# Optimization experiments

Hardware: AMD Instinct MI355X
Metric: run time of the kernel (lower is better)

The kernel has to match this reference:

```python
import jax, jax.numpy as jnp
import numpy as np

NUM_EXPERTS = 8
TOP_K = 2
HIDDEN = 1024
INTER_TOTAL = 8192  # intermediate_size * experts_per_rank
B, S = 2, 2048


def setup_inputs() -> dict:
    key = jax.random.key(0)
    k1, k2, k3, k4, k5, k6 = jax.random.split(key, 6)
    T = B * S
    x = jax.random.normal(k1, (B, S, HIDDEN), dtype=jnp.float32)
    scores = jax.random.uniform(k2, (T, NUM_EXPERTS), dtype=jnp.float32)
    expert_weights = jax.random.uniform(k3, (T, TOP_K), dtype=jnp.float32)
    top_experts = jax.random.randint(k4, (T, TOP_K), 0, NUM_EXPERTS, dtype=jnp.int32)
    w1 = jax.random.normal(k5, (HIDDEN, INTER_TOTAL), dtype=jnp.float32) * 0.02
    w2 = jax.random.normal(k6, (INTER_TOTAL, HIDDEN), dtype=jnp.float32) * 0.02
    return {"x": x, "scores": scores, "expert_weights": expert_weights,
            "top_experts": top_experts, "w1": w1, "w2": w2}


def reference(x, scores, expert_weights, top_experts, w1, w2):
    # forward_once with expert_parallel_size == 1 (dropless MoE dispatch/combine).
    in_shape = x.shape
    T = in_shape[0] * in_shape[1]
    H = in_shape[-1]
    x_flat = x.reshape(T, H)

    flat_experts = top_experts.reshape(-1)          # [T*top_k]
    flat_weights = expert_weights.reshape(-1)       # [T*top_k]

    # ops.sort: stable radix sort of routed copies by expert id
    order = jnp.argsort(flat_experts, stable=True)  # "indices"
    token_idx = order // TOP_K                      # source token per sorted slot

    # padded_gather: bucket tokens per expert (padding rows are zeros and
    # pass through the bias-free MLP as zeros, so they never affect output)
    xg = x_flat[token_idx]                          # [T*top_k, H]

    # MLP: w1 -> gelu(tanh approx) -> w2
    h = jax.nn.gelu(xg @ w1, approximate=True)      # [T*top_k, inter*E]
    y = h @ w2                                      # [T*top_k, H]

    # padded_scatter: weighted combine back to token order
    w_sorted = flat_weights[order]
    out = jnp.zeros((T, H), dtype=x.dtype).at[token_idx].add(w_sorted[:, None] * y)
    return out.reshape(in_shape)
```

## Files before the change

kernel.cpp:

```cpp
#include <hip/hip_runtime.h>
#include <hip/hip_bf16.h>
#include <math.h>

#define HID 1024
#define INTER 8192
#define TT 4096

typedef __bf16 bf16x8 __attribute__((ext_vector_type(8)));
typedef float f32x4 __attribute__((ext_vector_type(4)));

__device__ __forceinline__ void gll16(const void* g, void* l) {
    __builtin_amdgcn_global_load_lds(
        (const __attribute__((address_space(1))) void*)g,
        (__attribute__((address_space(3))) void*)l, 16, 0, 0);
}

template <int OFF>
__device__ __forceinline__ bf16x8 ds_read128o(unsigned addr) {
    bf16x8 r;
    asm volatile("ds_read_b128 %0, %1 offset:%c2" : "=v"(r) : "v"(addr), "i"(OFF));
    return r;
}

__global__ void k_prep(const float* __restrict__ x, const float* __restrict__ ew,
                       __hip_bfloat16* __restrict__ xb, float* __restrict__ s,
                       int n4, int T) {
    int stride = gridDim.x * blockDim.x;
    for (int i = blockIdx.x * blockDim.x + threadIdx.x; i < n4; i += stride) {
        float4 v = ((const float4*)x)[i];
        __hip_bfloat16* o = xb + (size_t)i * 4;
        o[0] = __float2bfloat16(v.x);
        o[1] = __float2bfloat16(v.y);
        o[2] = __float2bfloat16(v.z);
        o[3] = __float2bfloat16(v.w);
    }
    for (int t = blockIdx.x * blockDim.x + threadIdx.x; t < T; t += stride)
        s[t] = ew[2 * t] + ew[2 * t + 1];
}

__global__ void k_tcast(const float* __restrict__ in, __hip_bfloat16* __restrict__ out,
                        int R, int C) {
    __shared__ float tile[32][33];
    const int tx = threadIdx.x & 31, ty = threadIdx.x >> 5;
    const int br = blockIdx.y * 32, bc = blockIdx.x * 32;
#pragma unroll
    for (int j = 0; j < 32; j += 8)
        tile[ty + j][tx] = in[(size_t)(br + ty + j) * C + bc + tx];
    __syncthreads();
#pragma unroll
    for (int j = 0; j < 32; j += 8)
        out[(size_t)(bc + ty + j) * R + br + tx] = __float2bfloat16(tile[tx][ty + j]);
}

template <int EPI>
__global__ __launch_bounds__(512, 2) void k_gemm1b(
    const __hip_bfloat16* __restrict__ A, const __hip_bfloat16* __restrict__ Bt,
    __hip_bfloat16* __restrict__ hOut, float* __restrict__ fOut,
    const float* __restrict__ s, int Kfull, int nt, int Nout) {
    __shared__ __hip_bfloat16 sA[2][2][128][64];
    __shared__ __hip_bfloat16 sB[2][2][128][64];
    const int tid = threadIdx.x;
    const int lane = tid & 63, wid = tid >> 6;
    const int wr = wid >> 2, wc = wid & 3;

    const int nwg = gridDim.x * gridDim.y;
    const int wg = blockIdx.y * gridDim.x + blockIdx.x;
    const int swz = (wg & 7) * (nwg >> 3) + (wg >> 3);
    const int brow = (swz / gridDim.x) * 256;
    const int bcol = (swz % gridDim.x) * 256;
    const size_t kbase = (size_t)blockIdx.z * ((size_t)nt * 64);

    const int colsw = (((lane & 7) ^ (lane >> 3)) << 3);
    const int qA0 = (wid & 3) * 4;
    const int bh = (wid >> 1) & 1;
    const int qB0 = ((wid & 1) | ((wid >> 2) << 1)) * 4;
    const __hip_bfloat16* gA2 =
        A + (size_t)(brow + wr * 128 + qA0 * 8 + (lane >> 3)) * Kfull + kbase + colsw;
    const __hip_bfloat16* gB2 =
        Bt + (size_t)(bcol + bh * 128 + qB0 * 8 + (lane >> 3)) * Kfull + kbase + colsw;
    char* ldsA2 = (char*)&sA[0][0][0][0] + wr * 16384 + qA0 * 1024;
    char* ldsB2 = (char*)&sB[0][0][0][0] + bh * 16384 + qB0 * 1024;
    const size_t chunkStep = (size_t)8 * Kfull;

    const unsigned baseA = (unsigned)(uintptr_t)&sA[0][0][0][0];
    const unsigned baseB = (unsigned)(uintptr_t)&sB[0][0][0][0];
    const unsigned g0 = (((lane >> 4)) ^ (lane & 7)) << 4;
    const unsigned g1 = ((4 + (lane >> 4)) ^ (lane & 7)) << 4;
    const unsigned rdA0 = baseA + wr * 16384 + (lane & 15) * 128 + g0;
    const unsigned rdA1 = baseA + wr * 16384 + (lane & 15) * 128 + g1;
    const unsigned rdB0 = baseB + (wc >> 1) * 16384 + (wc & 1) * 8192 + (lane & 15) * 128 + g0;
    const unsigned rdB1 = baseB + (wc >> 1) * 16384 + (wc & 1) * 8192 + (lane & 15) * 128 + g1;

    f32x4 acc[8][4] = {};
    bf16x8 a03[4][2], a47[4][2], b01[2][2], b23[2][2];

#define STAGE_A2(bufoff, t)                                                    \
    do {                                                                       \
        _Pragma("unroll") for (int j = 0; j < 4; ++j)                          \
            gll16(gA2 + (size_t)j * chunkStep + (size_t)(t) * 64,              \
                  ldsA2 + (bufoff) + j * 1024);                                \
    } while (0)
#define STAGE_B2(bufoff, t)                                                    \
    do {                                                                       \
        _Pragma("unroll") for (int j = 0; j < 4; ++j)                          \
            gll16(gB2 + (size_t)j * chunkStep + (size_t)(t) * 64,              \
                  ldsB2 + (bufoff) + j * 1024);                                \
    } while (0)
#define PIN() __builtin_amdgcn_sched_barrier(0)
#define BAR()                              \
    do {                                   \
        PIN();                             \
        __builtin_amdgcn_s_barrier();      \
        PIN();                             \
    } while (0)
#define WAIT_LG12() __builtin_amdgcn_s_waitcnt(0xCC7F)
#define WAIT_LG8() __builtin_amdgcn_s_waitcnt(0xC87F)
#define WAIT_LG0() __builtin_amdgcn_s_waitcnt(0xC07F)
#define WAIT_VM0() __builtin_amdgcn_s_waitcnt(0x0F70)

    STAGE_A2(0u, 0);
    STAGE_B2(0u, 0);
    WAIT_VM0();
    BAR();

#pragma unroll 1
    for (int i = 0; i < nt; ++i) {
        const unsigned co = (i & 1) ? 32768u : 0u;
        const unsigned no = co ^ 32768u;
        const bool full = (i + 1 < nt);
        const unsigned aA0 = rdA0 + co, aA1 = rdA1 + co;
        const unsigned aB0 = rdB0 + co, aB1 = rdB1 + co;

        a03[0][0] = ds_read128o<0>(aA0);
        a03[0][1] = ds_read128o<0>(aA1);
        a03[1][0] = ds_read128o<2048>(aA0);
        a03[1][1] = ds_read128o<2048>(aA1);
        a03[2][0] = ds_read128o<4096>(aA0);
        a03[2][1] = ds_read128o<4096>(aA1);
        a03[3][0] = ds_read128o<6144>(aA0);
        a03[3][1] = ds_read128o<6144>(aA1);
        b01[0][0] = ds_read128o<0>(aB0);
        b01[0][1] = ds_read128o<0>(aB1);
        b01[1][0] = ds_read128o<2048>(aB0);
        b01[1][1] = ds_read128o<2048>(aB1);
        b23[0][0] = ds_read128o<4096>(aB0);
        b23[0][1] = ds_read128o<4096>(aB1);
        b23[1][0] = ds_read128o<6144>(aB0);
        b23[1][1] = ds_read128o<6144>(aB1);
        a47[0][0] = ds_read128o<8192>(aA0);
        a47[0][1] = ds_read128o<8192>(aA1);
        a47[1][0] = ds_read128o<10240>(aA0);
        a47[1][1] = ds_read128o<10240>(aA1);
        a47[2][0] = ds_read128o<12288>(aA0);
        a47[2][1] = ds_read128o<12288>(aA1);
        a47[3][0] = ds_read128o<14336>(aA0);
        a47[3][1] = ds_read128o<14336>(aA1);

        if (full) {
            STAGE_A2(no, i + 1);
            STAGE_B2(no, i + 1);
        }

        __builtin_amdgcn_s_setprio(1);
        WAIT_LG12();
        PIN();
#pragma unroll
        for (int ks = 0; ks < 2; ++ks)
#pragma unroll
            for (int m = 0; m < 4; ++m)
#pragma unroll
                for (int n = 0; n < 2; ++n)
                    acc[m][n] = __builtin_amdgcn_mfma_f32_16x16x32_bf16(
                        a03[m][ks], b01[n][ks], acc[m][n], 0, 0, 0);
        PIN();
        WAIT_LG8();
        PIN();
#pragma unroll
        for (int ks = 0; ks < 2; ++ks)
#pragma unroll
            for (int m = 0; m < 4; ++m)
#pragma unroll
                for (int n = 0; n < 2; ++n)
                    acc[m][2 + n] = __builtin_amdgcn_mfma_f32_16x16x32_bf16(
                        a03[m][ks], b23[n][ks], acc[m][2 + n], 0, 0, 0);
        PIN();
        WAIT_LG0();
        PIN();
#pragma unroll
        for (int ks = 0; ks < 2; ++ks)
#pragma unroll
            for (int m = 0; m < 4; ++m)
#pragma unroll
                for (int n = 0; n < 2; ++n)
                    acc[4 + m][2 + n] = __builtin_amdgcn_mfma_f32_16x16x32_bf16(
                        a47[m][ks], b23[n][ks], acc[4 + m][2 + n], 0, 0, 0);
#pragma unroll
        for (int ks = 0; ks < 2; ++ks)
#pragma unroll
            for (int m = 0; m < 4; ++m)
#pragma unroll
                for (int n = 0; n < 2; ++n)
                    acc[4 + m][n] = __builtin_amdgcn_mfma_f32_16x16x32_bf16(
                        a47[m][ks], b01[n][ks], acc[4 + m][n], 0, 0, 0);
        __builtin_amdgcn_s_setprio(0);
        PIN();
        WAIT_VM0();
        BAR();
    }

    const int orow = brow + wr * 128 + ((lane >> 4) << 2);
    const int ocol = bcol + wc * 64 + (lane & 15);
#pragma unroll
    for (int m = 0; m < 8; ++m) {
#pragma unroll
        for (int j = 0; j < 4; ++j) {
            const int r = orow + m * 16 + j;
            const size_t ro = (size_t)r * Nout;
            if (EPI == 0) {
#pragma unroll
                for (int n = 0; n < 4; ++n) {
                    float v = acc[m][n][j];
                    float u = 1.5957691216057308f * (v + 0.044715f * v * v * v);
                    float g = v / (1.0f + __expf(-u));
                    hOut[ro + ocol + n * 16] = __float2bfloat16(g);
                }
            } else {
                const float sc = s[r];
#pragma unroll
                for (int n = 0; n < 4; ++n)
                    unsafeAtomicAdd(&fOut[ro + ocol + n * 16], sc * acc[m][n][j]);
            }
        }
    }
#undef STAGE_A2
#undef STAGE_B2
#undef PIN
#undef BAR
#undef WAIT_LG12
#undef WAIT_LG8
#undef WAIT_LG0
#undef WAIT_VM0
}

extern "C" void kernel_launch(void* const* d_in, const int* in_sizes, int n_in,
                              void* d_out, int out_size, void* d_ws, size_t ws_size,
                              hipStream_t stream) {
    const float* x = (const float*)d_in[0];
    const float* ew = (const float*)d_in[2];
    const float* w1 = (const float*)d_in[4];
    const float* w2 = (const float*)d_in[5];
    float* out = (float*)d_out;

    char* ws = (char*)d_ws;
    float* s = (float*)ws;
    __hip_bfloat16* xb = (__hip_bfloat16*)(ws + 16384);
    __hip_bfloat16* w1t = (__hip_bfloat16*)(ws + 16384 + 8388608);
    __hip_bfloat16* w2t = (__hip_bfloat16*)(ws + 16384 + 8388608 + 16777216);
    __hip_bfloat16* h = (__hip_bfloat16*)(ws + 16384 + 8388608 + 2 * 16777216);

    k_prep<<<1024, 256, 0, stream>>>(x, ew, xb, s, (TT * HID) / 4, TT);

    dim3 t1(INTER / 32, HID / 32);
    k_tcast<<<t1, 256, 0, stream>>>(w1, w1t, HID, INTER);
    dim3 t2(HID / 32, INTER / 32);
    k_tcast<<<t2, 256, 0, stream>>>(w2, w2t, INTER, HID);

    dim3 g1(INTER / 256, TT / 256, 1);
    k_gemm1b<0><<<g1, 512, 0, stream>>>(xb, w1t, h, nullptr, nullptr, HID, HID / 64, INTER);

    hipMemsetAsync(out, 0, (size_t)TT * HID * sizeof(float), stream);
    dim3 g2(HID / 256, TT / 256, 4);
    k_gemm1b<1><<<g2, 512, 0, stream>>>(h, w2t, nullptr, out, s, INTER, 2048 / 64, HID);
}
```

Baseline: 202.5 us.

## Shrink GEMM block tile from 256x256 to 128x128 with 4 waves

Replaces the 256x256-tile, 8-wave GEMM kernel with a 128x128-tile, 4-wave variant used for both the up-projection and the down-projection (split-K) GEMMs. Each wave still computes a 64x64 sub-tile, LDS use per block is halved, and the grid has four times as many blocks. The goal is better load balance across CUs and more resident blocks. The cost is lower operand reuse per LDS byte, so more global and LDS traffic per FLOP.

Result: slower. 226.4 us (+11.8%).

```diff
diff --git a/kernel.cpp b/kernel.cpp
--- a/kernel.cpp
+++ b/kernel.cpp
@@ -53,55 +53,49 @@
 }
 
 template <int EPI>
-__global__ __launch_bounds__(512, 2) void k_gemm1b(
+__global__ __launch_bounds__(256, 2) void k_g128(
     const __hip_bfloat16* __restrict__ A, const __hip_bfloat16* __restrict__ Bt,
     __hip_bfloat16* __restrict__ hOut, float* __restrict__ fOut,
     const float* __restrict__ s, int Kfull, int nt, int Nout) {
-    __shared__ __hip_bfloat16 sA[2][2][128][64];
-    __shared__ __hip_bfloat16 sB[2][2][128][64];
+    __shared__ __hip_bfloat16 sA[2][128][64];
+    __shared__ __hip_bfloat16 sB[2][128][64];
     const int tid = threadIdx.x;
     const int lane = tid & 63, wid = tid >> 6;
-    const int wr = wid >> 2, wc = wid & 3;
+    const int wr = wid >> 1, wc = wid & 1;
 
     const int nwg = gridDim.x * gridDim.y;
     const int wg = blockIdx.y * gridDim.x + blockIdx.x;
     const int swz = (wg & 7) * (nwg >> 3) + (wg >> 3);
-    const int brow = (swz / gridDim.x) * 256;
-    const int bcol = (swz % gridDim.x) * 256;
+    const int brow = (swz / gridDim.x) * 128;
+    const int bcol = (swz % gridDim.x) * 128;
     const size_t kbase = (size_t)blockIdx.z * ((size_t)nt * 64);
 
     const int colsw = (((lane & 7) ^ (lane >> 3)) << 3);
-    const int qA0 = (wid & 3) * 4;
-    const int bh = (wid >> 1) & 1;
-    const int qB0 = ((wid & 1) | ((wid >> 2) << 1)) * 4;
     const __hip_bfloat16* gA2 =
-        A + (size_t)(brow + wr * 128 + qA0 * 8 + (lane >> 3)) * Kfull + kbase + colsw;
+        A + (size_t)(brow + wid * 32 + (lane >> 3)) * Kfull + kbase + colsw;
     const __hip_bfloat16* gB2 =
-        Bt + (size_t)(bcol + bh * 128 + qB0 * 8 + (lane >> 3)) * Kfull + kbase + colsw;
-    char* ldsA2 = (char*)&sA[0][0][0][0] + wr * 16384 + qA0 * 1024;
-    char* ldsB2 = (char*)&sB[0][0][0][0] + bh * 16384 + qB0 * 1024;
+        Bt + (size_t)(bcol + wid * 32 + (lane >> 3)) * Kfull + kbase + colsw;
+    char* ldsA2 = (char*)&sA[0][0][0] + wid * 4096;
+    char* ldsB2 = (char*)&sB[0][0][0] + wid * 4096;
     const size_t chunkStep = (size_t)8 * Kfull;
 
-    const unsigned baseA = (unsigned)(uintptr_t)&sA[0][0][0][0];
-    const unsigned baseB = (unsigned)(uintptr_t)&sB[0][0][0][0];
+    const unsigned baseA = (unsigned)(uintptr_t)&sA[0][0][0];
+    const unsigned baseB = (unsigned)(uintptr_t)&sB[0][0][0];
     const unsigned g0 = (((lane >> 4)) ^ (lane & 7)) << 4;
     const unsigned g1 = ((4 + (lane >> 4)) ^ (lane & 7)) << 4;
-    const unsigned rdA0 = baseA + wr * 16384 + (lane & 15) * 128 + g0;
-    const unsigned rdA1 = baseA + wr * 16384 + (lane & 15) * 128 + g1;
-    const unsigned rdB0 = baseB + (wc >> 1) * 16384 + (wc & 1) * 8192 + (lane & 15) * 128 + g0;
-    const unsigned rdB1 = baseB + (wc >> 1) * 16384 + (wc & 1) * 8192 + (lane & 15) * 128 + g1;
-
-    f32x4 acc[8][4] = {};
-    bf16x8 a03[4][2], a47[4][2], b01[2][2], b23[2][2];
-
-#define STAGE_A2(bufoff, t)                                                    \
+    const unsigned rdA0 = baseA + wr * 8192 + (lane & 15) * 128 + g0;
+    const unsigned rdA1 = baseA + wr * 8192 + (lane & 15) * 128 + g1;
+    const unsigned rdB0 = baseB + wc * 8192 + (lane & 15) * 128 + g0;
+    const unsigned rdB1 = baseB + wc * 8192 + (lane & 15) * 128 + g1;
+
+    f32x4 acc[4][4] = {};
+    bf16x8 aF[4][2], b01[2][2], b23[2][2];
+
+#define STAGE_AB(bufoff, t)                                                    \
     do {                                                                       \
         _Pragma("unroll") for (int j = 0; j < 4; ++j)                          \
             gll16(gA2 + (size_t)j * chunkStep + (size_t)(t) * 64,              \
                   ldsA2 + (bufoff) + j * 1024);                                \
-    } while (0)
-#define STAGE_B2(bufoff, t)                                                    \
-    do {                                                                       \
         _Pragma("unroll") for (int j = 0; j < 4; ++j)                          \
             gll16(gB2 + (size_t)j * chunkStep + (size_t)(t) * 64,              \
                   ldsB2 + (bufoff) + j * 1024);                                \
@@ -113,32 +107,30 @@
         __builtin_amdgcn_s_barrier();      \
         PIN();                             \
     } while (0)
-#define WAIT_LG12() __builtin_amdgcn_s_waitcnt(0xCC7F)
-#define WAIT_LG8() __builtin_amdgcn_s_waitcnt(0xC87F)
+#define WAIT_LG4() __builtin_amdgcn_s_waitcnt(0xC47F)
 #define WAIT_LG0() __builtin_amdgcn_s_waitcnt(0xC07F)
 #define WAIT_VM0() __builtin_amdgcn_s_waitcnt(0x0F70)
 
-    STAGE_A2(0u, 0);
-    STAGE_B2(0u, 0);
+    STAGE_AB(0u, 0);
     WAIT_VM0();
     BAR();
 
 #pragma unroll 1
     for (int i = 0; i < nt; ++i) {
-        const unsigned co = (i & 1) ? 32768u : 0u;
-        const unsigned no = co ^ 32768u;
+        const unsigned co = (i & 1) ? 16384u : 0u;
+        const unsigned no = co ^ 16384u;
         const bool full = (i + 1 < nt);
         const unsigned aA0 = rdA0 + co, aA1 = rdA1 + co;
         const unsigned aB0 = rdB0 + co, aB1 = rdB1 + co;
 
-        a03[0][0] = ds_read128o<0>(aA0);
-        a03[0][1] = ds_read128o<0>(aA1);
-        a03[1][0] = ds_read128o<2048>(aA0);
-        a03[1][1] = ds_read128o<2048>(aA1);
-        a03[2][0] = ds_read128o<4096>(aA0);
-        a03[2][1] = ds_read128o<4096>(aA1);
-        a03[3][0] = ds_read128o<6144>(aA0);
-        a03[3][1] = ds_read128o<6144>(aA1);
+        aF[0][0] = ds_read128o<0>(aA0);
+        aF[0][1] = ds_read128o<0>(aA1);
+        aF[1][0] = ds_read128o<2048>(aA0);
+        aF[1][1] = ds_read128o<2048>(aA1);
+        aF[2][0] = ds_read128o<4096>(aA0);
+        aF[2][1] = ds_read128o<4096>(aA1);
+        aF[3][0] = ds_read128o<6144>(aA0);
+        aF[3][1] = ds_read128o<6144>(aA1);
         b01[0][0] = ds_read128o<0>(aB0);
         b01[0][1] = ds_read128o<0>(aB1);
         b01[1][0] = ds_read128o<2048>(aB0);
@@ -147,22 +139,11 @@
         b23[0][1] = ds_read128o<4096>(aB1);
         b23[1][0] = ds_read128o<6144>(aB0);
         b23[1][1] = ds_read128o<6144>(aB1);
-        a47[0][0] = ds_read128o<8192>(aA0);
-        a47[0][1] = ds_read128o<8192>(aA1);
-        a47[1][0] = ds_read128o<10240>(aA0);
-        a47[1][1] = ds_read128o<10240>(aA1);
-        a47[2][0] = ds_read128o<12288>(aA0);
-        a47[2][1] = ds_read128o<12288>(aA1);
-        a47[3][0] = ds_read128o<14336>(aA0);
-        a47[3][1] = ds_read128o<14336>(aA1);
-
-        if (full) {
-            STAGE_A2(no, i + 1);
-            STAGE_B2(no, i + 1);
-        }
+
+        if (full) STAGE_AB(no, i + 1);
 
         __builtin_amdgcn_s_setprio(1);
-        WAIT_LG12();
+        WAIT_LG4();
         PIN();
 #pragma unroll
         for (int ks = 0; ks < 2; ++ks)
@@ -171,9 +152,9 @@
 #pragma unroll
                 for (int n = 0; n < 2; ++n)
                     acc[m][n] = __builtin_amdgcn_mfma_f32_16x16x32_bf16(
-                        a03[m][ks], b01[n][ks], acc[m][n], 0, 0, 0);
-        PIN();
-        WAIT_LG8();
+                        aF[m][ks], b01[n][ks], acc[m][n], 0, 0, 0);
+        PIN();
+        WAIT_LG0();
         PIN();
 #pragma unroll
         for (int ks = 0; ks < 2; ++ks)
@@ -182,36 +163,17 @@
 #pragma unroll
                 for (int n = 0; n < 2; ++n)
                     acc[m][2 + n] = __builtin_amdgcn_mfma_f32_16x16x32_bf16(
-                        a03[m][ks], b23[n][ks], acc[m][2 + n], 0, 0, 0);
-        PIN();
-        WAIT_LG0();
-        PIN();
-#pragma unroll
-        for (int ks = 0; ks < 2; ++ks)
-#pragma unroll
-            for (int m = 0; m < 4; ++m)
-#pragma unroll
-                for (int n = 0; n < 2; ++n)
-                    acc[4 + m][2 + n] = __builtin_amdgcn_mfma_f32_16x16x32_bf16(
-                        a47[m][ks], b23[n][ks], acc[4 + m][2 + n], 0, 0, 0);
-#pragma unroll
-        for (int ks = 0; ks < 2; ++ks)
-#pragma unroll
-            for (int m = 0; m < 4; ++m)
-#pragma unroll
-                for (int n = 0; n < 2; ++n)
-                    acc[4 + m][n] = __builtin_amdgcn_mfma_f32_16x16x32_bf16(
-                        a47[m][ks], b01[n][ks], acc[4 + m][n], 0, 0, 0);
+                        aF[m][ks], b23[n][ks], acc[m][2 + n], 0, 0, 0);
         __builtin_amdgcn_s_setprio(0);
         PIN();
         WAIT_VM0();
         BAR();
     }
 
-    const int orow = brow + wr * 128 + ((lane >> 4) << 2);
+    const int orow = brow + wr * 64 + ((lane >> 4) << 2);
     const int ocol = bcol + wc * 64 + (lane & 15);
 #pragma unroll
-    for (int m = 0; m < 8; ++m) {
+    for (int m = 0; m < 4; ++m) {
 #pragma unroll
         for (int j = 0; j < 4; ++j) {
             const int r = orow + m * 16 + j;
@@ -232,12 +194,10 @@
             }
         }
     }
-#undef STAGE_A2
-#undef STAGE_B2
+#undef STAGE_AB
 #undef PIN
 #undef BAR
-#undef WAIT_LG12
-#undef WAIT_LG8
+#undef WAIT_LG4
 #undef WAIT_LG0
 #undef WAIT_VM0
 }
@@ -265,10 +225,10 @@
     dim3 t2(HID / 32, INTER / 32);
     k_tcast<<<t2, 256, 0, stream>>>(w2, w2t, INTER, HID);
 
-    dim3 g1(INTER / 256, TT / 256, 1);
-    k_gemm1b<0><<<g1, 512, 0, stream>>>(xb, w1t, h, nullptr, nullptr, HID, HID / 64, INTER);
+    dim3 g1(INTER / 128, TT / 128, 1);
+    k_g128<0><<<g1, 256, 0, stream>>>(xb, w1t, h, nullptr, nullptr, HID, HID / 64, INTER);
 
     hipMemsetAsync(out, 0, (size_t)TT * HID * sizeof(float), stream);
-    dim3 g2(HID / 256, TT / 256, 4);
-    k_gemm1b<1><<<g2, 512, 0, stream>>>(h, w2t, nullptr, out, s, INTER, 2048 / 64, HID);
-}
+    dim3 g2(HID / 128, TT / 128, 4);
+    k_g128<1><<<g2, 256, 0, stream>>>(h, w2t, nullptr, out, s, INTER, 2048 / 64, HID);
+}
```
